# Optimization experiments

Measured on AMD Instinct MI355X. Metric: run time of the kernel, lower is better.

The kernel has to match this reference:

```python
import jax, jax.numpy as jnp
import numpy as np

T = 8192
INPUT = 1024
TRACE = 64
CTX = 16
OUT = 1024
EPS = 1e-5  # equinox LayerNorm default


def _linear(key, out_f, in_f):
    k1, k2 = jax.random.split(key)
    lim = 1.0 / np.sqrt(in_f)
    w = jax.random.uniform(k1, (out_f, in_f), minval=-lim, maxval=lim, dtype=jnp.float32)
    b = jax.random.uniform(k2, (out_f,), minval=-lim, maxval=lim, dtype=jnp.float32)
    return w, b


def setup_inputs() -> dict:
    key = jax.random.key(0)
    ks = jax.random.split(key, 8)
    x = jax.random.normal(ks[0], (T, INPUT), dtype=jnp.float32)
    start = jax.random.randint(ks[1], (T,), 0, 2).astype(bool)
    next_done = jax.random.randint(ks[2], (T,), 0, 2).astype(bool)
    state_re = jnp.zeros((1, TRACE, CTX), dtype=jnp.float32)
    state_im = jnp.zeros((1, TRACE, CTX), dtype=jnp.float32)
    pre_w, pre_b = _linear(ks[3], TRACE, INPUT)
    gi_w, gi_b = _linear(ks[4], TRACE, INPUT)
    go_w, go_b = _linear(ks[5], OUT, INPUT)
    skip_w, skip_b = _linear(ks[6], OUT, INPUT)
    mix_w, mix_b = _linear(ks[7], OUT, 2 * TRACE * CTX)
    # ffa.init: deterministic decay rates a and oscillation freqs b
    ffa_a = jnp.linspace(1e-6, 0.5, TRACE, dtype=jnp.float32)
    ffa_b = (2.0 * jnp.pi / jnp.exp(jnp.linspace(jnp.log(1.0), jnp.log(1024.0), CTX))).astype(jnp.float32)
    return dict(x=x, state_re=state_re, state_im=state_im, start=start, next_done=next_done,
                pre_w=pre_w, pre_b=pre_b, gi_w=gi_w, gi_b=gi_b, go_w=go_w, go_b=go_b,
                skip_w=skip_w, skip_b=skip_b, mix_w=mix_w, mix_b=mix_b,
                ffa_a=ffa_a, ffa_b=ffa_b)


def _ffa_apply(ffa_a, ffa_b, gated_x, state0, start):
    """Resettable complex linear recurrence: s_t = gamma * s_{t-1} + x_t, reset at episode starts.
    gamma = exp(-|a| + i b), outer over (trace, context). Parallelized with an associative scan
    over monoid elements (reset_flag, state, elapsed_steps)."""
    Tn, m = gated_x.shape
    c = ffa_b.shape[0]
    ab = jax.lax.complex(
        jnp.broadcast_to(-jnp.abs(ffa_a)[None, :, None], (1, m, c)),
        jnp.broadcast_to(ffa_b[None, None, :], (1, m, c)),
    )  # [1, m, c] complex: log-gamma per unit timestep

    xc = jnp.broadcast_to(gated_x[:, :, None].astype(jnp.complex64), (Tn, m, c))
    # prepend carried-in recurrent state: timestep 0, no reset
    x_e = jnp.concatenate([state0.astype(jnp.complex64), xc], axis=0)          # [T+1, m, c]
    s_e = jnp.concatenate([jnp.zeros((1, 1, 1), bool), start[:, None, None]], axis=0)
    i_e = jnp.concatenate([jnp.zeros((1, 1, 1), jnp.float32),
                           jnp.ones((Tn, 1, 1), jnp.float32)], axis=0)

    def op(a, b):
        s1, x1, i1 = a
        s2, x2, i2 = b
        # zero the carried state across episode boundaries
        x1 = jnp.where(s2, 0.0, x1)
        i1 = jnp.where(s2, 0.0, i1)
        g = jnp.exp(ab * i2.astype(jnp.complex64))  # decay over i2 elapsed steps
        return (jnp.logical_or(s1, s2), x1 * g + x2, i1 + i2)

    _, states, _ = jax.lax.associative_scan(op, (s_e, x_e, i_e), axis=0)
    return states[1:]  # [T, m, c] complex64


def reference(x, state_re, state_im, start, next_done,
              pre_w, pre_b, gi_w, gi_b, go_w, go_b,
              skip_w, skip_b, mix_w, mix_b, ffa_a, ffa_b):
    gate_in = jax.nn.sigmoid(x @ gi_w.T + gi_b)          # [T, trace]
    pre = x @ pre_w.T + pre_b                            # [T, trace]
    gated_x = pre * gate_in

    state0 = jax.lax.complex(state_re, state_im)         # [1, trace, ctx]
    state = _ffa_apply(ffa_a, ffa_b, gated_x, state0, start)  # [T, trace, ctx] complex

    z_in = jnp.concatenate([jnp.real(state), jnp.imag(state)], axis=-1)
    z_in = z_in.reshape(state.shape[0], -1)              # [T, 2*trace*ctx]
    z = z_in @ mix_w.T + mix_b                           # [T, out]

    gate_out = jax.nn.sigmoid(x @ go_w.T + go_b)         # [T, out]
    skip = x @ skip_w.T + skip_b                         # [T, out]

    zg = z * gate_out
    mu = zg.mean(-1, keepdims=True)
    var = ((zg - mu) ** 2).mean(-1, keepdims=True)
    ln = (zg - mu) / jnp.sqrt(var + EPS)                 # LayerNorm, no affine

    out = ln + skip * (1.0 - gate_out)
    final_state = state[-1:]
    return out, final_state


if __name__ == "__main__":
    inp = setup_inputs()
    out, fs = jax.jit(reference)(**inp)
    print(out.shape, out.dtype, fs.shape, fs.dtype)
```

## Files before the change

### kernel.cpp

```cpp
#include <hip/hip_runtime.h>
#include <math.h>

#define T_DIM 8192
#define IN_DIM 1024
#define TRACE 64
#define CTX 16
#define OUT_DIM 1024
#define KMIX 2048

typedef __attribute__((ext_vector_type(8))) short bf16x8;
typedef __attribute__((ext_vector_type(4))) float f32x4;
typedef __attribute__((ext_vector_type(16))) float f32x16;

__device__ __forceinline__ unsigned short f2bf(float f) {
    unsigned int u = __float_as_uint(f);
    u = (u + 0x7FFFu + ((u >> 16) & 1u)) >> 16;
    return (unsigned short)u;
}
__device__ __forceinline__ float bf2f(unsigned short b) {
    return __uint_as_float(((unsigned int)b) << 16);
}

__device__ __forceinline__ void gl2lds16(const void* g, void* l) {
    __builtin_amdgcn_global_load_lds(
        (const __attribute__((address_space(1))) unsigned int*)g,
        (__attribute__((address_space(3))) unsigned int*)l,
        16, 0, 0);
}


__global__ __launch_bounds__(256) void c0_conv(const float* __restrict__ x,
        const float* __restrict__ gw, const float* __restrict__ sw, const float* __restrict__ mw,
        const float* __restrict__ pw, const float* __restrict__ giw,
        const void* __restrict__ startp,
        unsigned short* __restrict__ xb, unsigned short* __restrict__ gob,
        unsigned short* __restrict__ skb, unsigned short* __restrict__ mixb,
        unsigned short* __restrict__ pwb, unsigned short* __restrict__ gwb,
        unsigned char* __restrict__ mask)
{
    if (blockIdx.x == 0) {
        __shared__ int nonbool;
        int tid = threadIdx.x;
        if (tid == 0) nonbool = 0;
        __syncthreads();
        const unsigned int* wv = (const unsigned int*)startp;
        #pragma unroll
        for (int p = 0; p < 8; p++) {
            unsigned int a = wv[tid * 8 + p];
            if (a > 1u) nonbool = 1;
        }
        __syncthreads();
        if (nonbool) {
            const unsigned char* s8 = (const unsigned char*)startp;
            for (int i = tid; i < T_DIM; i += 256) mask[i] = (unsigned char)(s8[i] != 0);
        } else {
            const int* s32 = (const int*)startp;
            for (int i = tid; i < T_DIM; i += 256) mask[i] = (unsigned char)(s32[i] != 0);
        }
    }
    const size_t QX = 2097152, QG = 262144, QS = 262144, QM = 524288, QP = 16384, QI = 16384;
    const size_t total = QX + QG + QS + QM + QP + QI;
    for (size_t q = (size_t)blockIdx.x * blockDim.x + threadIdx.x; q < total;
         q += (size_t)gridDim.x * blockDim.x) {
        const float* src; unsigned short* dst; size_t i;
        if (q < QX)                  { src = x;   dst = xb;   i = q; }
        else if (q < QX+QG)          { src = gw;  dst = gob;  i = q - QX; }
        else if (q < QX+QG+QS)       { src = sw;  dst = skb;  i = q - QX - QG; }
        else if (q < QX+QG+QS+QM)    { src = mw;  dst = mixb; i = q - QX - QG - QS; }
        else if (q < QX+QG+QS+QM+QP) { src = pw;  dst = pwb;  i = q - QX - QG - QS - QM; }
        else                         { src = giw; dst = gwb;  i = q - QX - QG - QS - QM - QP; }
        float4 v = *(const float4*)(src + i * 4);
        ushort4 o;
        o.x = f2bf(v.x); o.y = f2bf(v.y); o.z = f2bf(v.z); o.w = f2bf(v.w);
        *(ushort4*)(dst + i * 4) = o;
    }
}

__global__ __launch_bounds__(256) void k1_mfma(const unsigned short* __restrict__ xb,
        const unsigned short* __restrict__ pwb, const unsigned short* __restrict__ gwb,
        const float* __restrict__ pre_b, const float* __restrict__ gi_b,
        float* __restrict__ gxT)
{
    __shared__ __align__(16) unsigned short As[1024];
    __shared__ __align__(16) unsigned short Bs[4096];
    __shared__ float sgE[64][33];

    const int tid = threadIdx.x;
    const int t0 = blockIdx.x * 32;
    const int lane = tid & 63, w = tid >> 6;
    const int quad = lane >> 4, l16 = lane & 15;
    const int r = tid >> 2, s4 = tid & 3;
    const int csw = (s4 - ((r >> 1) & 3)) & 3;

    f32x4 acc[2][2];
    const f32x4 zero4 = {0.f, 0.f, 0.f, 0.f};
    #pragma unroll
    for (int mi = 0; mi < 2; mi++)
        #pragma unroll
        for (int ni = 0; ni < 2; ni++) acc[mi][ni] = zero4;

    const int sfr = (quad + ((l16 >> 1) & 3)) & 3;

    for (int k0 = 0; k0 < IN_DIM; k0 += 32) {
        __syncthreads();
        if (tid < 128) {
            int ra = tid >> 2;
            int ca = ((tid & 3) - ((ra >> 1) & 3)) & 3;
            gl2lds16(xb + (size_t)(t0 + ra) * IN_DIM + k0 + ca * 8, As + tid * 8);
        }
        gl2lds16(pwb + (size_t)r * IN_DIM + k0 + csw * 8, Bs + tid * 8);
        gl2lds16(gwb + (size_t)r * IN_DIM + k0 + csw * 8, Bs + 2048 + tid * 8);
        asm volatile("s_waitcnt vmcnt(0)" ::: "memory");
        __syncthreads();
        bf16x8 af[2], bf[2];
        #pragma unroll
        for (int mi = 0; mi < 2; mi++)
            af[mi] = *(const bf16x8*)&As[(mi * 16 + l16) * 32 + sfr * 8];
        #pragma unroll
        for (int ni = 0; ni < 2; ni++)
            bf[ni] = *(const bf16x8*)&Bs[(w * 32 + ni * 16 + l16) * 32 + sfr * 8];
        #pragma unroll
        for (int mi = 0; mi < 2; mi++)
            #pragma unroll
            for (int ni = 0; ni < 2; ni++)
                acc[mi][ni] = __builtin_amdgcn_mfma_f32_16x16x32_bf16(af[mi], bf[ni], acc[mi][ni], 0, 0, 0);
    }

    if (w >= 2) {
        #pragma unroll
        for (int mi = 0; mi < 2; mi++)
            #pragma unroll
            for (int ni = 0; ni < 2; ni++) {
                int mg = (w - 2) * 32 + ni * 16 + l16;
                float gb = gi_b[mg];
                #pragma unroll
                for (int rr = 0; rr < 4; rr++) {
                    int tl = mi * 16 + quad * 4 + rr;
                    sgE[mg][tl] = 1.f / (1.f + expf(-(acc[mi][ni][rr] + gb)));
                }
            }
    }
    __syncthreads();
    if (w < 2) {
        #pragma unroll
        for (int mi = 0; mi < 2; mi++)
            #pragma unroll
            for (int ni = 0; ni < 2; ni++) {
                int mp = w * 32 + ni * 16 + l16;
                float pb = pre_b[mp];
                float4 o;
                float* po = &o.x;
                #pragma unroll
                for (int rr = 0; rr < 4; rr++) {
                    int tl = mi * 16 + quad * 4 + rr;
                    po[rr] = (acc[mi][ni][rr] + pb) * sgE[mp][tl];
                }
                *(float4*)&gxT[(size_t)mp * T_DIM + t0 + mi * 16 + quad * 4] = o;
            }
    }
}

__global__ __launch_bounds__(128) void k2_scan(const float* __restrict__ gxT,
        const unsigned char* __restrict__ mask8,
        const float* __restrict__ state_re, const float* __restrict__ state_im,
        const float* __restrict__ ffa_a, const float* __restrict__ ffa_b,
        unsigned short* __restrict__ zinTb, float* __restrict__ fstate)
{
    const int m = blockIdx.x >> 4;
    const int c = blockIdx.x & 15;
    const int j = threadIdx.x;
    __shared__ float Br[128], Bi[128], Er[128], Ei[128];
    __shared__ unsigned char Rf[128];
    __shared__ unsigned int SB[128 * 33];

    const float am = -fabsf(ffa_a[m]);
    const float bc = ffa_b[c];
    const float er = expf(am);
    const float gr = er * cosf(bc);
    const float gi = er * sinf(bc);

    const float* gx = gxT + (size_t)m * T_DIM;
    const int t0 = j * 64;

    unsigned long long rmask = 0ull;
    float sre = 0.f, sim = 0.f;
    bool r = false;
    #pragma unroll 8
    for (int i = 0; i < 64; i++) {
        int t = t0 + i;
        if (mask8[t]) { rmask |= 1ull << i; sre = 0.f; sim = 0.f; r = true; }
        else { float tr_ = sre * gr - sim * gi; sim = sre * gi + sim * gr; sre = tr_; }
        sre += gx[t];
    }
    Br[j] = sre; Bi[j] = sim; Rf[j] = r ? 1 : 0;
    __syncthreads();
    if (j == 0) {
        float e64  = expf(64.f * am);
        float g64r = e64 * cosf(64.f * bc);
        float g64i = e64 * sinf(64.f * bc);
        float pr = state_re[m * CTX + c], pi = state_im[m * CTX + c];
        for (int q = 0; q < 128; q++) {
            Er[q] = pr; Ei[q] = pi;
            if (Rf[q]) { pr = Br[q]; pi = Bi[q]; }
            else {
                float nr = pr * g64r - pi * g64i + Br[q];
                pi       = pr * g64i + pi * g64r + Bi[q];
                pr = nr;
            }
        }
    }
    __syncthreads();
    sre = Er[j]; sim = Ei[j];
    unsigned int ore[32], oim[32];
    #pragma unroll
    for (int i = 0; i < 64; i++) {
        int t = t0 + i;
        if (rmask & (1ull << i)) { sre = 0.f; sim = 0.f; }
        else { float tr_ = sre * gr - sim * gi; sim = sre * gi + sim * gr; sre = tr_; }
        sre += gx[t];
        unsigned short hr = f2bf(sre), hi_ = f2bf(sim);
        if (i & 1) { ore[i >> 1] |= ((unsigned int)hr) << 16; oim[i >> 1] |= ((unsigned int)hi_) << 16; }
        else       { ore[i >> 1]  = hr;                        oim[i >> 1]  = hi_; }
    }
    if (j == 127) {
        int p = m * CTX + c;
        fstate[p]        = sre;
        fstate[1024 + p] = sim;
    }

    unsigned short* zreb = zinTb + (size_t)(m * 32 + c)      * T_DIM;
    unsigned short* zimb = zinTb + (size_t)(m * 32 + 16 + c) * T_DIM;

    #pragma unroll
    for (int q = 0; q < 32; q++) SB[j * 33 + q] = ore[q];
    __syncthreads();
    #pragma unroll
    for (int it = 0; it < 8; it++) {
        int g = (it * 128 + j) * 4;
        int jj = g >> 5, qq = g & 31;
        uint4 v = *(uint4*)&SB[jj * 33 + qq];
        *(uint4*)(zreb + g * 2) = v;
    }
    __syncthreads();
    #pragma unroll
    for (int q = 0; q < 32; q++) SB[j * 33 + q] = oim[q];
    __syncthreads();
    #pragma unroll
    for (int it = 0; it < 8; it++) {
        int g = (it * 128 + j) * 4;
        int jj = g >> 5, qq = g & 31;
        uint4 v = *(uint4*)&SB[jj * 33 + qq];
        *(uint4*)(zimb + g * 2) = v;
    }
}

__global__ __launch_bounds__(256) void t3_tr(const unsigned short* __restrict__ zinTb,
                                             unsigned short* __restrict__ zinb)
{
    __shared__ unsigned short S[64][72];
    const int k0 = blockIdx.x * 64, t0 = blockIdx.y * 64;
    const int tid = threadIdx.x;
    {
        int kr = tid >> 3, tc = (tid & 7) * 8;
        #pragma unroll
        for (int p = 0; p < 2; p++) {
            int k = kr + p * 32;
            ushort4 a = *(const ushort4*)&zinTb[(size_t)(k0 + k) * T_DIM + t0 + tc];
            ushort4 b = *(const ushort4*)&zinTb[(size_t)(k0 + k) * T_DIM + t0 + tc + 4];
            *(ushort4*)&S[k][tc]     = a;
            *(ushort4*)&S[k][tc + 4] = b;
        }
    }
    __syncthreads();
    {
        int tr = tid >> 3, kc = (tid & 7) * 8;
        #pragma unroll
        for (int p = 0; p < 2; p++) {
            int t = tr + p * 32;
            ushort4 o1, o2;
            o1.x = S[kc+0][t]; o1.y = S[kc+1][t]; o1.z = S[kc+2][t]; o1.w = S[kc+3][t];
            o2.x = S[kc+4][t]; o2.y = S[kc+5][t]; o2.z = S[kc+6][t]; o2.w = S[kc+7][t];
            *(ushort4*)&zinb[(size_t)(t0 + t) * KMIX + k0 + kc]     = o1;
            *(ushort4*)&zinb[(size_t)(t0 + t) * KMIX + k0 + kc + 4] = o2;
        }
    }
}

__global__ __launch_bounds__(512, 2) void gA_gemm(
        const unsigned short* __restrict__ xb,   const unsigned short* __restrict__ zinb,
        const unsigned short* __restrict__ gob,  const unsigned short* __restrict__ skb,
        const unsigned short* __restrict__ mixb,
        const float* __restrict__ go_b, const float* __restrict__ skip_b, const float* __restrict__ mix_b,
        unsigned short* __restrict__ zg, unsigned short* __restrict__ sk2)
{
    __shared__ __align__(16) unsigned short L[49152];
    const int tid = threadIdx.x;
    const int b = blockIdx.x;
    const int xcd = b & 7, q = b >> 3;
    const int t0 = (xcd * 4 + (q >> 3)) * 256;
    const int n0 = (q & 7) * 128;

    const int lane = tid & 63, w = tid >> 6;
    const int wm = w >> 1, wn = w & 1;
    const int l31 = lane & 31, h = lane >> 5;
    const int r = tid >> 2;
    const int csw = ((tid & 3) - ((r >> 1) & 3)) & 3;
    const int c8 = csw * 8;
    const int srot = (l31 >> 1) & 3;
    const int dst8 = tid * 8;

    f32x16 accg[2][2], acck[2][2];
    #pragma unroll
    for (int mi = 0; mi < 2; mi++)
        #pragma unroll
        for (int ni = 0; ni < 2; ni++)
            #pragma unroll
            for (int e = 0; e < 16; e++) { accg[mi][ni][e] = 0.f; acck[mi][ni][e] = 0.f; }

    {
        const unsigned short* gA0 = xb  + (size_t)(t0 + r)       * IN_DIM + c8;
        const unsigned short* gA1 = xb  + (size_t)(t0 + 128 + r) * IN_DIM + c8;
        const unsigned short* gB0 = gob + (size_t)(n0 + r)       * IN_DIM + c8;
        const unsigned short* gC0 = skb + (size_t)(n0 + r)       * IN_DIM + c8;

#define STAGE_F(bufi, kof) do {                         \
        unsigned short* _b = &L[(bufi) * 16384];        \
        gl2lds16(gA0 + (kof), _b + dst8);               \
        gl2lds16(gA1 + (kof), _b + 4096 + dst8);        \
        gl2lds16(gB0 + (kof), _b + 8192 + dst8);        \
        gl2lds16(gC0 + (kof), _b + 12288 + dst8);       \
    } while (0)

        STAGE_F(0, 0);
        STAGE_F(1, 32);
        asm volatile("s_waitcnt vmcnt(4)" ::: "memory");
        __builtin_amdgcn_s_barrier();

        int cur = 0, nx2 = 2;
        for (int t = 0; t < 32; ++t) {
            const unsigned short* As = &L[cur * 16384];
            const unsigned short* Bs = As + 8192;
            const unsigned short* Cs = As + 12288;
            const bool st = (t + 2 < 32);
            #pragma unroll
            for (int kh = 0; kh < 2; kh++) {
                const int so = ((kh * 2 + h + srot) & 3) * 8;
                bf16x8 af[2], bg[2], bk[2];
                #pragma unroll
                for (int mi = 0; mi < 2; mi++)
                    af[mi] = *(const bf16x8*)&As[(wm * 64 + mi * 32 + l31) * 32 + so];
                #pragma unroll
                for (int ni = 0; ni < 2; ni++) {
                    bg[ni] = *(const bf16x8*)&Bs[(wn * 64 + ni * 32 + l31) * 32 + so];
                    bk[ni] = *(const bf16x8*)&Cs[(wn * 64 + ni * 32 + l31) * 32 + so];
                }
                if (kh == 0 && st) STAGE_F(nx2, (t + 2) * 32);
                __builtin_amdgcn_s_setprio(1);
                #pragma unroll
                for (int mi = 0; mi < 2; mi++)
                    #pragma unroll
                    for (int ni = 0; ni < 2; ni++) {
                        accg[mi][ni] = __builtin_amdgcn_mfma_f32_32x32x16_bf16(af[mi], bg[ni], accg[mi][ni], 0, 0, 0);
                        acck[mi][ni] = __builtin_amdgcn_mfma_f32_32x32x16_bf16(af[mi], bk[ni], acck[mi][ni], 0, 0, 0);
                    }
                __builtin_amdgcn_s_setprio(0);
            }
            if (st) { asm volatile("s_waitcnt vmcnt(4)" ::: "memory"); }
            else    { asm volatile("s_waitcnt vmcnt(0)" ::: "memory"); }
            __builtin_amdgcn_s_barrier();
            cur = (cur == 2) ? 0 : cur + 1;
            nx2 = (nx2 == 2) ? 0 : nx2 + 1;
        }
#undef STAGE_F
    }

    unsigned int sigp[32];
    #pragma unroll
    for (int mi = 0; mi < 2; mi++)
        #pragma unroll
        for (int ni = 0; ni < 2; ni++) {
            int n = n0 + wn * 64 + ni * 32 + l31;
            float gb = go_b[n];
            float sb_ = skip_b[n];
            #pragma unroll
            for (int reg = 0; reg < 16; reg++) {
                int row = (reg & 3) + 8 * (reg >> 2) + 4 * h;
                int t = t0 + wm * 64 + mi * 32 + row;
                float s = 1.f / (1.f + expf(-(accg[mi][ni][reg] + gb)));
                sk2[(size_t)t * OUT_DIM + n] = f2bf((acck[mi][ni][reg] + sb_) * (1.f - s));
                unsigned int pk = (unsigned int)f2bf(s);
                int idx = (mi * 2 + ni) * 8 + (reg >> 1);
                if (reg & 1) sigp[idx] |= pk << 16;
                else         sigp[idx]  = pk;
            }
        }

    #pragma unroll
    for (int mi = 0; mi < 2; mi++)
        #pragma unroll
        for (int ni = 0; ni < 2; ni++)
            #pragma unroll
            for (int e = 0; e < 16; e++) accg[mi][ni][e] = 0.f;
    {
        const unsigned short* mA0 = zinb + (size_t)(t0 + r)       * KMIX + c8;
        const unsigned short* mA1 = zinb + (size_t)(t0 + 128 + r) * KMIX + c8;
        const unsigned short* mB0 = mixb + (size_t)(n0 + r)       * KMIX + c8;

#define STAGE_M(bufi, kof) do {                         \
        unsigned short* _b = &L[(bufi) * 16384];        \
        gl2lds16(mA0 + (kof), _b + dst8);               \
        gl2lds16(mA1 + (kof), _b + 4096 + dst8);        \
        gl2lds16(mB0 + (kof), _b + 8192 + dst8);        \
    } while (0)

        STAGE_M(0, 0);
        STAGE_M(1, 32);
        asm volatile("s_waitcnt vmcnt(3)" ::: "memory");
        __builtin_amdgcn_s_barrier();

        int cur = 0, nx2 = 2;
        for (int t = 0; t < 64; ++t) {
            const unsigned short* As = &L[cur * 16384];
            const unsigned short* Bs = As + 8192;
            const bool st = (t + 2 < 64);
            #pragma unroll
            for (int kh = 0; kh < 2; kh++) {
                const int so = ((kh * 2 + h + srot) & 3) * 8;
                bf16x8 af[2], bf[2];
                #pragma unroll
                for (int mi = 0; mi < 2; mi++)
                    af[mi] = *(const bf16x8*)&As[(wm * 64 + mi * 32 + l31) * 32 + so];
                #pragma unroll
                for (int ni = 0; ni < 2; ni++)
                    bf[ni] = *(const bf16x8*)&Bs[(wn * 64 + ni * 32 + l31) * 32 + so];
                if (kh == 0 && st) STAGE_M(nx2, (t + 2) * 32);
                __builtin_amdgcn_s_setprio(1);
                #pragma unroll
                for (int mi = 0; mi < 2; mi++)
                    #pragma unroll
                    for (int ni = 0; ni < 2; ni++)
                        accg[mi][ni] = __builtin_amdgcn_mfma_f32_32x32x16_bf16(af[mi], bf[ni], accg[mi][ni], 0, 0, 0);
                __builtin_amdgcn_s_setprio(0);
            }
            if (st) { asm volatile("s_waitcnt vmcnt(3)" ::: "memory"); }
            else    { asm volatile("s_waitcnt vmcnt(0)" ::: "memory"); }
            __builtin_amdgcn_s_barrier();
            cur = (cur == 2) ? 0 : cur + 1;
            nx2 = (nx2 == 2) ? 0 : nx2 + 1;
        }
#undef STAGE_M
    }

    #pragma unroll
    for (int mi = 0; mi < 2; mi++)
        #pragma unroll
        for (int ni = 0; ni < 2; ni++) {
            int n = n0 + wn * 64 + ni * 32 + l31;
            float mb_ = mix_b[n];
            #pragma unroll
            for (int reg = 0; reg < 16; reg++) {
                int row = (reg & 3) + 8 * (reg >> 2) + 4 * h;
                int t = t0 + wm * 64 + mi * 32 + row;
                unsigned int u = sigp[(mi * 2 + ni) * 8 + (reg >> 1)];
                float sig = bf2f((unsigned short)((reg & 1) ? (u >> 16) : (u & 0xffff)));
                zg[(size_t)t * OUT_DIM + n] = f2bf((accg[mi][ni][reg] + mb_) * sig);
            }
        }
}

__global__ __launch_bounds__(256) void g3_ln(const unsigned short* __restrict__ zg,
        const unsigned short* __restrict__ sk2, float* __restrict__ out)
{
    __shared__ float sb[4], qb[4];
    __shared__ float mu_s, rstd_s;
    const int t = blockIdx.x;
    const int tid = threadIdx.x;
    ushort4 zu = *(const ushort4*)&zg [(size_t)t * OUT_DIM + tid * 4];
    ushort4 su = *(const ushort4*)&sk2[(size_t)t * OUT_DIM + tid * 4];
    float z0 = bf2f(zu.x), z1 = bf2f(zu.y), z2 = bf2f(zu.z), z3 = bf2f(zu.w);
    float s0 = bf2f(su.x), s1 = bf2f(su.y), s2 = bf2f(su.z), s3 = bf2f(su.w);
    float s = z0 + z1 + z2 + z3;
    float q = z0*z0 + z1*z1 + z2*z2 + z3*z3;
    #pragma unroll
    for (int off = 32; off > 0; off >>= 1) {
        s += __shfl_down(s, off, 64);
        q += __shfl_down(q, off, 64);
    }
    int wid = tid >> 6;
    if ((tid & 63) == 0) { sb[wid] = s; qb[wid] = q; }
    __syncthreads();
    if (tid == 0) {
        float S = sb[0] + sb[1] + sb[2] + sb[3];
        float Q = qb[0] + qb[1] + qb[2] + qb[3];
        float mu = S * (1.f / 1024.f);
        float var = Q * (1.f / 1024.f) - mu * mu;
        mu_s = mu; rstd_s = rsqrtf(var + 1e-5f);
    }
    __syncthreads();
    float mu = mu_s, rs = rstd_s;
    float4 o;
    o.x = (z0 - mu) * rs + s0;
    o.y = (z1 - mu) * rs + s1;
    o.z = (z2 - mu) * rs + s2;
    o.w = (z3 - mu) * rs + s3;
    *(float4*)&out[(size_t)t * OUT_DIM + tid * 4] = o;
}

__global__ void g4_final(const float* __restrict__ fstate, float* __restrict__ out, int out_size)
{
    int i = blockIdx.x * blockDim.x + threadIdx.x;
    if (i >= 2048) return;
    long long base = (long long)T_DIM * OUT_DIM;
    if (base + i < (long long)out_size) out[base + i] = fstate[i];
}

extern "C" void kernel_launch(void* const* d_in, const int* in_sizes, int n_in,
                              void* d_out, int out_size, void* d_ws, size_t ws_size,
                              hipStream_t stream) {
    const float* x        = (const float*)d_in[0];
    const float* state_re = (const float*)d_in[1];
    const float* state_im = (const float*)d_in[2];
    const void*  startp   = d_in[3];
    const float* pre_w    = (const float*)d_in[5];
    const float* pre_b    = (const float*)d_in[6];
    const float* gi_w     = (const float*)d_in[7];
    const float* gi_b     = (const float*)d_in[8];
    const float* go_w     = (const float*)d_in[9];
    const float* go_b     = (const float*)d_in[10];
    const float* skip_w   = (const float*)d_in[11];
    const float* skip_b   = (const float*)d_in[12];
    const float* mix_w    = (const float*)d_in[13];
    const float* mix_b    = (const float*)d_in[14];
    const float* ffa_a    = (const float*)d_in[15];
    const float* ffa_b    = (const float*)d_in[16];

    float* ws = (float*)d_ws;
    float*          gxT    = ws;
    unsigned short* zinTb  = (unsigned short*)(ws + 524288);
    unsigned short* zinb   = (unsigned short*)(ws + 8912896);
    unsigned short* xb     = (unsigned short*)(ws + 17301504);
    unsigned short* gob    = (unsigned short*)(ws + 21495808);
    unsigned short* skb    = (unsigned short*)(ws + 22020096);
    unsigned short* mixb   = (unsigned short*)(ws + 22544384);
    unsigned short* zg     = (unsigned short*)(ws + 23592960);
    unsigned short* sk2    = (unsigned short*)(ws + 27787264);
    float*          fstate = ws + 31981568;
    unsigned char*  mask   = (unsigned char*)(ws + 31983616);
    unsigned short* pwb    = zg;
    unsigned short* gwb    = zg + 65536;
    float* out = (float*)d_out;

    hipLaunchKernelGGL(c0_conv,  dim3(1536),    dim3(256),  0, stream, x, go_w, skip_w, mix_w, pre_w, gi_w,
                                                             startp, xb, gob, skb, mixb, pwb, gwb, mask);
    hipLaunchKernelGGL(k1_mfma,  dim3(256),     dim3(256),  0, stream, xb, pwb, gwb, pre_b, gi_b, gxT);
    hipLaunchKernelGGL(k2_scan,  dim3(1024),    dim3(128),  0, stream, gxT, mask, state_re, state_im, ffa_a, ffa_b, zinTb, fstate);
    hipLaunchKernelGGL(t3_tr,    dim3(32, 128), dim3(256),  0, stream, zinTb, zinb);
    hipLaunchKernelGGL(gA_gemm,  dim3(256),     dim3(512),  0, stream, xb, zinb, gob, skb, mixb, go_b, skip_b, mix_b, zg, sk2);
    hipLaunchKernelGGL(g3_ln,    dim3(8192),    dim3(256),  0, stream, zg, sk2, out);
    hipLaunchKernelGGL(g4_final, dim3(8),       dim3(256),  0, stream, fstate, out, out_size);
}
```

Baseline: 296.9 us.

## Shrink fused GEMM tiles to 128x64 with 1024 blocks and double buffering

The fused gate/skip/mix GEMM kernel moves from 256x128 tiles with 512 threads and triple-buffered LDS to 128x64 tiles with 256 threads, double buffering and four blocks per CU, launching 1024 blocks instead of 256. Each wave now computes a 64x32 sub-tile. The first mix-GEMM stage is issued before the sigmoid/skip epilogue so its load overlaps that work. The aim is better CU occupancy and load balance across the device; the cost is less operand reuse per tile, more global and LDS traffic, and a full vmcnt(0) wait every iteration, which limits how much load latency is hidden.

New measurement: 323.9 us. +9.1%, slower.

```diff
diff --git a/kernel.cpp b/kernel.cpp
--- a/kernel.cpp
+++ b/kernel.cpp
@@ -286,19 +286,19 @@
     }
 }
 
-__global__ __launch_bounds__(512, 2) void gA_gemm(
+__global__ __launch_bounds__(256, 4) void gA_gemm(
         const unsigned short* __restrict__ xb,   const unsigned short* __restrict__ zinb,
         const unsigned short* __restrict__ gob,  const unsigned short* __restrict__ skb,
         const unsigned short* __restrict__ mixb,
         const float* __restrict__ go_b, const float* __restrict__ skip_b, const float* __restrict__ mix_b,
         unsigned short* __restrict__ zg, unsigned short* __restrict__ sk2)
 {
-    __shared__ __align__(16) unsigned short L[49152];
+    __shared__ __align__(16) unsigned short L[16384];
     const int tid = threadIdx.x;
     const int b = blockIdx.x;
     const int xcd = b & 7, q = b >> 3;
-    const int t0 = (xcd * 4 + (q >> 3)) * 256;
-    const int n0 = (q & 7) * 128;
+    const int t0 = (xcd * 8 + (q >> 4)) * 128;
+    const int n0 = (q & 15) * 64;
 
     const int lane = tid & 63, w = tid >> 6;
     const int wm = w >> 1, wn = w & 1;
@@ -309,163 +309,133 @@
     const int srot = (l31 >> 1) & 3;
     const int dst8 = tid * 8;
 
-    f32x16 accg[2][2], acck[2][2];
+    f32x16 accg[2], acck[2];
     #pragma unroll
     for (int mi = 0; mi < 2; mi++)
         #pragma unroll
-        for (int ni = 0; ni < 2; ni++)
-            #pragma unroll
-            for (int e = 0; e < 16; e++) { accg[mi][ni][e] = 0.f; acck[mi][ni][e] = 0.f; }
+        for (int e = 0; e < 16; e++) { accg[mi][e] = 0.f; acck[mi][e] = 0.f; }
 
     {
-        const unsigned short* gA0 = xb  + (size_t)(t0 + r)       * IN_DIM + c8;
-        const unsigned short* gA1 = xb  + (size_t)(t0 + 128 + r) * IN_DIM + c8;
-        const unsigned short* gB0 = gob + (size_t)(n0 + r)       * IN_DIM + c8;
-        const unsigned short* gC0 = skb + (size_t)(n0 + r)       * IN_DIM + c8;
+        const unsigned short* gA0 = xb  + (size_t)(t0 + r)      * IN_DIM + c8;
+        const unsigned short* gA1 = xb  + (size_t)(t0 + 64 + r) * IN_DIM + c8;
+        const unsigned short* gB0 = gob + (size_t)(n0 + r)      * IN_DIM + c8;
+        const unsigned short* gC0 = skb + (size_t)(n0 + r)      * IN_DIM + c8;
 
 #define STAGE_F(bufi, kof) do {                         \
-        unsigned short* _b = &L[(bufi) * 16384];        \
+        unsigned short* _b = &L[(bufi) * 8192];         \
         gl2lds16(gA0 + (kof), _b + dst8);               \
-        gl2lds16(gA1 + (kof), _b + 4096 + dst8);        \
-        gl2lds16(gB0 + (kof), _b + 8192 + dst8);        \
-        gl2lds16(gC0 + (kof), _b + 12288 + dst8);       \
+        gl2lds16(gA1 + (kof), _b + 2048 + dst8);        \
+        gl2lds16(gB0 + (kof), _b + 4096 + dst8);        \
+        gl2lds16(gC0 + (kof), _b + 6144 + dst8);        \
     } while (0)
 
         STAGE_F(0, 0);
-        STAGE_F(1, 32);
-        asm volatile("s_waitcnt vmcnt(4)" ::: "memory");
+        asm volatile("s_waitcnt vmcnt(0)" ::: "memory");
         __builtin_amdgcn_s_barrier();
 
-        int cur = 0, nx2 = 2;
         for (int t = 0; t < 32; ++t) {
-            const unsigned short* As = &L[cur * 16384];
-            const unsigned short* Bs = As + 8192;
-            const unsigned short* Cs = As + 12288;
-            const bool st = (t + 2 < 32);
+            if (t + 1 < 32) STAGE_F((t + 1) & 1, (t + 1) * 32);
+            const unsigned short* As = &L[(t & 1) * 8192];
+            const unsigned short* Bs = As + 4096;
+            const unsigned short* Cs = As + 6144;
             #pragma unroll
             for (int kh = 0; kh < 2; kh++) {
                 const int so = ((kh * 2 + h + srot) & 3) * 8;
-                bf16x8 af[2], bg[2], bk[2];
-                #pragma unroll
-                for (int mi = 0; mi < 2; mi++)
-                    af[mi] = *(const bf16x8*)&As[(wm * 64 + mi * 32 + l31) * 32 + so];
-                #pragma unroll
-                for (int ni = 0; ni < 2; ni++) {
-                    bg[ni] = *(const bf16x8*)&Bs[(wn * 64 + ni * 32 + l31) * 32 + so];
-                    bk[ni] = *(const bf16x8*)&Cs[(wn * 64 + ni * 32 + l31) * 32 + so];
-                }
-                if (kh == 0 && st) STAGE_F(nx2, (t + 2) * 32);
+                bf16x8 af0 = *(const bf16x8*)&As[(wm * 64 + l31) * 32 + so];
+                bf16x8 af1 = *(const bf16x8*)&As[(wm * 64 + 32 + l31) * 32 + so];
+                bf16x8 bg  = *(const bf16x8*)&Bs[(wn * 32 + l31) * 32 + so];
+                bf16x8 bk  = *(const bf16x8*)&Cs[(wn * 32 + l31) * 32 + so];
                 __builtin_amdgcn_s_setprio(1);
-                #pragma unroll
-                for (int mi = 0; mi < 2; mi++)
-                    #pragma unroll
-                    for (int ni = 0; ni < 2; ni++) {
-                        accg[mi][ni] = __builtin_amdgcn_mfma_f32_32x32x16_bf16(af[mi], bg[ni], accg[mi][ni], 0, 0, 0);
-                        acck[mi][ni] = __builtin_amdgcn_mfma_f32_32x32x16_bf16(af[mi], bk[ni], acck[mi][ni], 0, 0, 0);
-                    }
+                accg[0] = __builtin_amdgcn_mfma_f32_32x32x16_bf16(af0, bg, accg[0], 0, 0, 0);
+                acck[0] = __builtin_amdgcn_mfma_f32_32x32x16_bf16(af0, bk, acck[0], 0, 0, 0);
+                accg[1] = __builtin_amdgcn_mfma_f32_32x32x16_bf16(af1, bg, accg[1], 0, 0, 0);
+                acck[1] = __builtin_amdgcn_mfma_f32_32x32x16_bf16(af1, bk, acck[1], 0, 0, 0);
                 __builtin_amdgcn_s_setprio(0);
             }
-            if (st) { asm volatile("s_waitcnt vmcnt(4)" ::: "memory"); }
-            else    { asm volatile("s_waitcnt vmcnt(0)" ::: "memory"); }
+            asm volatile("s_waitcnt vmcnt(0)" ::: "memory");
             __builtin_amdgcn_s_barrier();
-            cur = (cur == 2) ? 0 : cur + 1;
-            nx2 = (nx2 == 2) ? 0 : nx2 + 1;
         }
 #undef STAGE_F
     }
 
-    unsigned int sigp[32];
-    #pragma unroll
-    for (int mi = 0; mi < 2; mi++)
-        #pragma unroll
-        for (int ni = 0; ni < 2; ni++) {
-            int n = n0 + wn * 64 + ni * 32 + l31;
-            float gb = go_b[n];
-            float sb_ = skip_b[n];
+    const unsigned short* mA0 = zinb + (size_t)(t0 + r)      * KMIX + c8;
+    const unsigned short* mA1 = zinb + (size_t)(t0 + 64 + r) * KMIX + c8;
+    const unsigned short* mB0 = mixb + (size_t)(n0 + r)      * KMIX + c8;
+
+#define STAGE_M(bufi, kof) do {                         \
+        unsigned short* _b = &L[(bufi) * 8192];         \
+        gl2lds16(mA0 + (kof), _b + dst8);               \
+        gl2lds16(mA1 + (kof), _b + 2048 + dst8);        \
+        gl2lds16(mB0 + (kof), _b + 4096 + dst8);        \
+    } while (0)
+
+    STAGE_M(0, 0);
+
+    unsigned int sigp[16];
+    {
+        const int n = n0 + wn * 32 + l31;
+        const float gb = go_b[n];
+        const float sb_ = skip_b[n];
+        #pragma unroll
+        for (int mi = 0; mi < 2; mi++) {
             #pragma unroll
             for (int reg = 0; reg < 16; reg++) {
                 int row = (reg & 3) + 8 * (reg >> 2) + 4 * h;
                 int t = t0 + wm * 64 + mi * 32 + row;
-                float s = 1.f / (1.f + expf(-(accg[mi][ni][reg] + gb)));
-                sk2[(size_t)t * OUT_DIM + n] = f2bf((acck[mi][ni][reg] + sb_) * (1.f - s));
+                float s = 1.f / (1.f + expf(-(accg[mi][reg] + gb)));
+                sk2[(size_t)t * OUT_DIM + n] = f2bf((acck[mi][reg] + sb_) * (1.f - s));
                 unsigned int pk = (unsigned int)f2bf(s);
-                int idx = (mi * 2 + ni) * 8 + (reg >> 1);
+                int idx = mi * 8 + (reg >> 1);
                 if (reg & 1) sigp[idx] |= pk << 16;
                 else         sigp[idx]  = pk;
             }
         }
+    }
 
     #pragma unroll
     for (int mi = 0; mi < 2; mi++)
         #pragma unroll
-        for (int ni = 0; ni < 2; ni++)
-            #pragma unroll
-            for (int e = 0; e < 16; e++) accg[mi][ni][e] = 0.f;
+        for (int e = 0; e < 16; e++) accg[mi][e] = 0.f;
     {
-        const unsigned short* mA0 = zinb + (size_t)(t0 + r)       * KMIX + c8;
-        const unsigned short* mA1 = zinb + (size_t)(t0 + 128 + r) * KMIX + c8;
-        const unsigned short* mB0 = mixb + (size_t)(n0 + r)       * KMIX + c8;
-
-#define STAGE_M(bufi, kof) do {                         \
-        unsigned short* _b = &L[(bufi) * 16384];        \
-        gl2lds16(mA0 + (kof), _b + dst8);               \
-        gl2lds16(mA1 + (kof), _b + 4096 + dst8);        \
-        gl2lds16(mB0 + (kof), _b + 8192 + dst8);        \
-    } while (0)
-
-        STAGE_M(0, 0);
-        STAGE_M(1, 32);
-        asm volatile("s_waitcnt vmcnt(3)" ::: "memory");
+        asm volatile("s_waitcnt vmcnt(0)" ::: "memory");
         __builtin_amdgcn_s_barrier();
 
-        int cur = 0, nx2 = 2;
         for (int t = 0; t < 64; ++t) {
-            const unsigned short* As = &L[cur * 16384];
-            const unsigned short* Bs = As + 8192;
-            const bool st = (t + 2 < 64);
+            if (t + 1 < 64) STAGE_M((t + 1) & 1, (t + 1) * 32);
+            const unsigned short* As = &L[(t & 1) * 8192];
+            const unsigned short* Bs = As + 4096;
             #pragma unroll
             for (int kh = 0; kh < 2; kh++) {
                 const int so = ((kh * 2 + h + srot) & 3) * 8;
-                bf16x8 af[2], bf[2];
-                #pragma unroll
-                for (int mi = 0; mi < 2; mi++)
-                    af[mi] = *(const bf16x8*)&As[(wm * 64 + mi * 32 + l31) * 32 + so];
-                #pragma unroll
-                for (int ni = 0; ni < 2; ni++)
-                    bf[ni] = *(const bf16x8*)&Bs[(wn * 64 + ni * 32 + l31) * 32 + so];
-                if (kh == 0 && st) STAGE_M(nx2, (t + 2) * 32);
+                bf16x8 af0 = *(const bf16x8*)&As[(wm * 64 + l31) * 32 + so];
+                bf16x8 af1 = *(const bf16x8*)&As[(wm * 64 + 32 + l31) * 32 + so];
+                bf16x8 bf  = *(const bf16x8*)&Bs[(wn * 32 + l31) * 32 + so];
                 __builtin_amdgcn_s_setprio(1);
-                #pragma unroll
-                for (int mi = 0; mi < 2; mi++)
-                    #pragma unroll
-                    for (int ni = 0; ni < 2; ni++)
-                        accg[mi][ni] = __builtin_amdgcn_mfma_f32_32x32x16_bf16(af[mi], bf[ni], accg[mi][ni], 0, 0, 0);
+                accg[0] = __builtin_amdgcn_mfma_f32_32x32x16_bf16(af0, bf, accg[0], 0, 0, 0);
+                accg[1] = __builtin_amdgcn_mfma_f32_32x32x16_bf16(af1, bf, accg[1], 0, 0, 0);
                 __builtin_amdgcn_s_setprio(0);
             }
-            if (st) { asm volatile("s_waitcnt vmcnt(3)" ::: "memory"); }
-            else    { asm volatile("s_waitcnt vmcnt(0)" ::: "memory"); }
+            asm volatile("s_waitcnt vmcnt(0)" ::: "memory");
             __builtin_amdgcn_s_barrier();
-            cur = (cur == 2) ? 0 : cur + 1;
-            nx2 = (nx2 == 2) ? 0 : nx2 + 1;
         }
 #undef STAGE_M
     }
 
-    #pragma unroll
-    for (int mi = 0; mi < 2; mi++)
-        #pragma unroll
-        for (int ni = 0; ni < 2; ni++) {
-            int n = n0 + wn * 64 + ni * 32 + l31;
-            float mb_ = mix_b[n];
+    {
+        const int n = n0 + wn * 32 + l31;
+        const float mb_ = mix_b[n];
+        #pragma unroll
+        for (int mi = 0; mi < 2; mi++) {
             #pragma unroll
             for (int reg = 0; reg < 16; reg++) {
                 int row = (reg & 3) + 8 * (reg >> 2) + 4 * h;
                 int t = t0 + wm * 64 + mi * 32 + row;
-                unsigned int u = sigp[(mi * 2 + ni) * 8 + (reg >> 1)];
+                unsigned int u = sigp[mi * 8 + (reg >> 1)];
                 float sig = bf2f((unsigned short)((reg & 1) ? (u >> 16) : (u & 0xffff)));
-                zg[(size_t)t * OUT_DIM + n] = f2bf((accg[mi][ni][reg] + mb_) * sig);
-            }
-        }
+                zg[(size_t)t * OUT_DIM + n] = f2bf((accg[mi][reg] + mb_) * sig);
+            }
+        }
+    }
 }
 
 __global__ __launch_bounds__(256) void g3_ln(const unsigned short* __restrict__ zg,
@@ -555,7 +525,7 @@
     hipLaunchKernelGGL(k1_mfma,  dim3(256),     dim3(256),  0, stream, xb, pwb, gwb, pre_b, gi_b, gxT);
     hipLaunchKernelGGL(k2_scan,  dim3(1024),    dim3(128),  0, stream, gxT, mask, state_re, state_im, ffa_a, ffa_b, zinTb, fstate);
     hipLaunchKernelGGL(t3_tr,    dim3(32, 128), dim3(256),  0, stream, zinTb, zinb);
-    hipLaunchKernelGGL(gA_gemm,  dim3(256),     dim3(512),  0, stream, xb, zinb, gob, skb, mixb, go_b, skip_b, mix_b, zg, sk2);
+    hipLaunchKernelGGL(gA_gemm,  dim3(1024),    dim3(256),  0, stream, xb, zinb, gob, skb, mixb, go_b, skip_b, mix_b, zg, sk2);
     hipLaunchKernelGGL(g3_ln,    dim3(8192),    dim3(256),  0, stream, zg, sk2, out);
     hipLaunchKernelGGL(g4_final, dim3(8),       dim3(256),  0, stream, fstate, out, out_size);
 }
```
